# Kernel tuning notes

Measured on AMD Instinct MI355X. Metric: run time of the kernel, lower is better.

Reference implementation:

```python
import jax, jax.numpy as jnp
import numpy as np

N, E, H, C = 50000, 1_600_000, 4, 32
DIN, DE = 128, 32
NEG_SLOPE = 0.2  # PyG GATConv leaky_relu negative_slope default


def setup_inputs() -> dict:
    key = jax.random.key(0)
    ks = jax.random.split(key, 12)
    s = 0.1  # weight scale
    return {
        "x": jax.random.normal(ks[0], (N, DIN), jnp.float32),
        "edge_index": jax.random.randint(ks[1], (2, E), 0, N, jnp.int32),
        "edge_attr": jax.random.normal(ks[2], (E, DE), jnp.float32),
        "W": jax.random.normal(ks[3], (DIN, H * C), jnp.float32) * s,
        "att_src": jax.random.normal(ks[4], (H, C), jnp.float32) * s,
        "att_dst": jax.random.normal(ks[5], (H, C), jnp.float32) * s,
        "lin_edge_W": jax.random.normal(ks[6], (DE, H * C), jnp.float32) * s,
        "att_edge": jax.random.normal(ks[7], (H, C), jnp.float32) * s,
        "bias": jax.random.normal(ks[8], (H * C,), jnp.float32) * s,
        "proj_W": jax.random.normal(ks[9], (H * C, C), jnp.float32) * s,
        "proj_b": jax.random.normal(ks[10], (C,), jnp.float32) * s,
    }


def reference(x, edge_index, edge_attr, W, att_src, att_dst, lin_edge_W,
              att_edge, bias, proj_W, proj_b):
    n = x.shape[0]
    h, c = att_src.shape
    src, dst = edge_index[0], edge_index[1]

    # add self loops; loop edge_attr = mean of incoming edge_attr (PyG fill_value='mean')
    deg = jax.ops.segment_sum(jnp.ones(src.shape, x.dtype), dst, num_segments=n)
    ea_mean = jax.ops.segment_sum(edge_attr, dst, num_segments=n) / jnp.maximum(deg, 1.0)[:, None]
    loop = jnp.arange(n, dtype=src.dtype)
    src = jnp.concatenate([src, loop])
    dst = jnp.concatenate([dst, loop])
    ea = jnp.concatenate([edge_attr, ea_mean], axis=0)

    xl = (x @ W).reshape(n, h, c)                       # [N,H,C]
    a_src = jnp.einsum('nhc,hc->nh', xl, att_src)       # [N,H]
    a_dst = jnp.einsum('nhc,hc->nh', xl, att_dst)
    e = (ea @ lin_edge_W).reshape(-1, h, c)             # [E',H,C]
    a_e = jnp.einsum('ehc,hc->eh', e, att_edge)

    alpha = jax.nn.leaky_relu(a_src[src] + a_dst[dst] + a_e, NEG_SLOPE)  # [E',H]
    amax = jax.lax.stop_gradient(jax.ops.segment_max(alpha, dst, num_segments=n))
    alpha = jnp.exp(alpha - amax[dst])
    denom = jax.ops.segment_sum(alpha, dst, num_segments=n)
    alpha = alpha / (denom[dst] + 1e-16)                # segment softmax over incoming edges

    out = jax.ops.segment_sum(xl[src] * alpha[..., None], dst, num_segments=n)  # [N,H,C]
    out = out.reshape(n, h * c) + bias                  # concat heads + bias
    return out @ proj_W + proj_b                        # concat projection
```

## Files before the change

kernel.cpp:

```cpp
#include <hip/hip_runtime.h>

#define NEG_SLOPE 0.2f

__device__ __forceinline__ float lrelu(float x) { return x > 0.0f ? x : NEG_SLOPE * x; }

__device__ __forceinline__ float bcast(float v, int srcLane) {
  return __int_as_float(__builtin_amdgcn_readlane(__float_as_int(v), srcLane));
}

__device__ __forceinline__ unsigned pack_bf16(float a, float b) {
  unsigned ua = __float_as_uint(a), ub = __float_as_uint(b);
  ua += 0x7fffu + ((ua >> 16) & 1u);
  ub += 0x7fffu + ((ub >> 16) & 1u);
  return (ua >> 16) | (ub & 0xffff0000u);
}
__device__ __forceinline__ float bf16lo(unsigned z) { return __uint_as_float(z << 16); }
__device__ __forceinline__ float bf16hi(unsigned z) { return __uint_as_float(z & 0xffff0000u); }

__global__ void k0_setup(const float* __restrict__ W, const float* __restrict__ proj_W,
                         const float* __restrict__ att_src, const float* __restrict__ att_dst,
                         const float* __restrict__ lin_edge_W, const float* __restrict__ att_edge,
                         const float* __restrict__ bias, const float* __restrict__ proj_b,
                         float* __restrict__ Wz, float* __restrict__ Ws, float* __restrict__ Wd,
                         float* __restrict__ M, float* __restrict__ cproj) {
  int t = blockIdx.x * blockDim.x + threadIdx.x;
  if (t < 16384) {
    int d = t >> 7, o = t & 127;
    int h = o >> 5, jj = o & 31;
    float s = 0.f;
    #pragma unroll
    for (int c = 0; c < 32; ++c)
      s += W[d * 128 + h * 32 + c] * proj_W[(h * 32 + c) * 32 + jj];
    Wz[d * 128 + o] = s;
  } else if (t < 16384 + 512) {
    int idx = t - 16384; int d = idx >> 2, h = idx & 3;
    float s = 0.f;
    #pragma unroll
    for (int c = 0; c < 32; ++c) s += W[d * 128 + h * 32 + c] * att_src[h * 32 + c];
    Ws[d * 4 + h] = s;
  } else if (t < 16384 + 1024) {
    int idx = t - 16384 - 512; int d = idx >> 2, h = idx & 3;
    float s = 0.f;
    #pragma unroll
    for (int c = 0; c < 32; ++c) s += W[d * 128 + h * 32 + c] * att_dst[h * 32 + c];
    Wd[d * 4 + h] = s;
  } else if (t < 16384 + 1024 + 128) {
    int idx = t - 16384 - 1024; int d = idx >> 2, h = idx & 3;
    float s = 0.f;
    #pragma unroll
    for (int c = 0; c < 32; ++c) s += lin_edge_W[d * 128 + h * 32 + c] * att_edge[h * 32 + c];
    M[d * 4 + h] = s;
  } else if (t < 16384 + 1024 + 128 + 32) {
    int jj = t - 16384 - 1024 - 128;
    float s = proj_b[jj];
    #pragma unroll
    for (int k = 0; k < 128; ++k) s += bias[k] * proj_W[k * 32 + jj];
    cproj[jj] = s;
  }
}

__global__ __launch_bounds__(256) void k3_gemm(
    const float* __restrict__ x, const float* __restrict__ Wz,
    const float* __restrict__ Ws, const float* __restrict__ Wd,
    int n, unsigned* __restrict__ Zp, float* __restrict__ a_src, float* __restrict__ a_dst) {
  __shared__ float2 Wl[128 * 64];
  int tid = threadIdx.x;
  for (int idx = tid; idx < 128 * 64; idx += 256) {
    int k = idx >> 6, l = idx & 63;
    Wl[idx] = make_float2(Wz[k * 128 + l], Wz[k * 128 + 64 + l]);
  }
  __syncthreads();
  int lane = tid & 63, wid = tid >> 6;
  float ws0[4], ws1[4], wd0[4], wd1[4];
  #pragma unroll
  for (int h = 0; h < 4; ++h) {
    ws0[h] = Ws[lane * 4 + h];  ws1[h] = Ws[(64 + lane) * 4 + h];
    wd0[h] = Wd[lane * 4 + h];  wd1[h] = Wd[(64 + lane) * 4 + h];
  }
  int gw = blockIdx.x * 4 + wid;
  int nw = gridDim.x * 4;
  for (int base = gw * 4; base < n; base += nw * 4) {
    float xa[4], xb[4];
    #pragma unroll
    for (int u = 0; u < 4; ++u) {
      int node = base + u;
      xa[u] = (node < n) ? x[node * 128 + lane] : 0.0f;
      xb[u] = (node < n) ? x[node * 128 + 64 + lane] : 0.0f;
    }
    float acc0[4] = {0.f, 0.f, 0.f, 0.f}, acc1[4] = {0.f, 0.f, 0.f, 0.f};
    #pragma unroll 16
    for (int k = 0; k < 64; ++k) {
      float2 w = Wl[k * 64 + lane];
      #pragma unroll
      for (int u = 0; u < 4; ++u) {
        float xv = bcast(xa[u], k);
        acc0[u] += xv * w.x; acc1[u] += xv * w.y;
      }
    }
    #pragma unroll 16
    for (int k = 0; k < 64; ++k) {
      float2 w = Wl[(64 + k) * 64 + lane];
      #pragma unroll
      for (int u = 0; u < 4; ++u) {
        float xv = bcast(xb[u], k);
        acc0[u] += xv * w.x; acc1[u] += xv * w.y;
      }
    }
    #pragma unroll
    for (int u = 0; u < 4; ++u) {
      int node = base + u;
      if (node >= n) break;
      Zp[(size_t)node * 64 + lane] = pack_bf16(acc0[u], acc1[u]);
      float ps[4], pd[4];
      #pragma unroll
      for (int h = 0; h < 4; ++h) {
        ps[h] = xa[u] * ws0[h] + xb[u] * ws1[h];
        pd[h] = xa[u] * wd0[h] + xb[u] * wd1[h];
      }
      #pragma unroll
      for (int m = 1; m < 64; m <<= 1) {
        #pragma unroll
        for (int h = 0; h < 4; ++h) {
          ps[h] += __shfl_xor(ps[h], m);
          pd[h] += __shfl_xor(pd[h], m);
        }
      }
      if (lane == 0) {
        *(float4*)&a_src[node * 4] = make_float4(ps[0], ps[1], ps[2], ps[3]);
        *(float4*)&a_dst[node * 4] = make_float4(pd[0], pd[1], pd[2], pd[3]);
      }
    }
  }
}

__global__ __launch_bounds__(256) void k1_edge(
    const int* __restrict__ ei, int E, const float4* __restrict__ ea4,
    const float* __restrict__ Mg,
    const float* __restrict__ a_src, const float* __restrict__ a_dst,
    uint4* __restrict__ we, int* __restrict__ deg, int* __restrict__ rank) {
  int lane = threadIdx.x & 63, wid = threadIdx.x >> 6;
  int j = lane & 7;
  const float4* Mf4 = (const float4*)Mg;
  float4 m0 = Mf4[4 * j + 0], m1 = Mf4[4 * j + 1];
  float4 m2 = Mf4[4 * j + 2], m3 = Mf4[4 * j + 3];
  int perm = 8 * (lane & 7) + (lane >> 3);
  int gw = blockIdx.x * 4 + wid, nw = gridDim.x * 4;
  int ntiles = (E + 63) >> 6;
  for (int tile = gw; tile < ntiles; tile += nw) {
    int T0 = tile << 6;
    size_t fbase = (size_t)T0 * 8;
    float cx = 0.f, cy = 0.f, cz = 0.f, cw = 0.f;
    #pragma unroll
    for (int k = 0; k < 8; ++k) {
      size_t idx = fbase + (size_t)k * 64 + lane;
      float4 v = (idx < (size_t)E * 8) ? ea4[idx] : make_float4(0.f, 0.f, 0.f, 0.f);
      float px = v.x * m0.x + v.y * m1.x + v.z * m2.x + v.w * m3.x;
      float py = v.x * m0.y + v.y * m1.y + v.z * m2.y + v.w * m3.y;
      float pz = v.x * m0.z + v.y * m1.z + v.z * m2.z + v.w * m3.z;
      float pw = v.x * m0.w + v.y * m1.w + v.z * m2.w + v.w * m3.w;
      #pragma unroll
      for (int m = 1; m < 8; m <<= 1) {
        px += __shfl_xor(px, m); py += __shfl_xor(py, m);
        pz += __shfl_xor(pz, m); pw += __shfl_xor(pw, m);
      }
      if (j == k) { cx = px; cy = py; cz = pz; cw = pw; }
    }
    int e = T0 + perm;
    if (e < E) {
      int s = ei[e], d = ei[E + e];
      int rk = atomicAdd(&deg[d], 1);
      float4 as = *(const float4*)&a_src[(size_t)s * 4];
      float4 ad = *(const float4*)&a_dst[(size_t)d * 4];
      float w0 = __expf(lrelu(cx + as.x + ad.x));
      float w1 = __expf(lrelu(cy + as.y + ad.y));
      float w2 = __expf(lrelu(cz + as.z + ad.z));
      float w3 = __expf(lrelu(cw + as.w + ad.w));
      we[e] = make_uint4(pack_bf16(w0, w1), pack_bf16(w2, w3),
                         pack_bf16(cx, cy), pack_bf16(cz, cw));
      rank[e] = rk;
    }
  }
}

__global__ void k2_scan(const int* __restrict__ deg, int n, int* __restrict__ offsets) {
  __shared__ int shw[16];
  __shared__ int shtot;
  int tid = threadIdx.x;
  int lane = tid & 63, wid = tid >> 6;
  int running = 0;
  for (int base = 0; base < n; base += 4096) {
    int i = base + tid * 4;
    int4 v = make_int4(0, 0, 0, 0);
    if (i + 3 < n) v = *(const int4*)&deg[i];
    else {
      if (i < n) v.x = deg[i];
      if (i + 1 < n) v.y = deg[i + 1];
      if (i + 2 < n) v.z = deg[i + 2];
      if (i + 3 < n) v.w = deg[i + 3];
    }
    int tsum = v.x + v.y + v.z + v.w;
    int inc = tsum;
    #pragma unroll
    for (int s = 1; s < 64; s <<= 1) {
      int t = __shfl_up(inc, s);
      if (lane >= s) inc += t;
    }
    if (lane == 63) shw[wid] = inc;
    __syncthreads();
    if (wid == 0) {
      int w = (lane < 16) ? shw[lane] : 0;
      int winc = w;
      #pragma unroll
      for (int s = 1; s < 16; s <<= 1) {
        int t = __shfl_up(winc, s);
        if (lane >= s) winc += t;
      }
      if (lane < 16) shw[lane] = winc - w;
      if (lane == 15) shtot = winc;
    }
    __syncthreads();
    int excl = running + shw[wid] + inc - tsum;
    if (i < n)     offsets[i + 1] = excl + v.x;
    if (i + 1 < n) offsets[i + 2] = excl + v.x + v.y;
    if (i + 2 < n) offsets[i + 3] = excl + v.x + v.y + v.z;
    if (i + 3 < n) offsets[i + 4] = excl + tsum;
    running += shtot;
    __syncthreads();
  }
  if (tid == 0) offsets[0] = 0;
}

__global__ void k4_scatter(const int* __restrict__ ei, int E,
                           const int* __restrict__ rank, const int* __restrict__ offsets,
                           const uint4* __restrict__ we, uint4* __restrict__ csr) {
  int e = blockIdx.x * blockDim.x + threadIdx.x;
  if (e >= E) return;
  int s = ei[e], d = ei[E + e];
  int slot = offsets[d] + rank[e];
  uint4 w = we[e];
  uint4* ent = &csr[(size_t)slot * 2];
  *(int*)ent = s;
  ent[1] = w;
}

__global__ __launch_bounds__(256) void k5_agg(
    const int* __restrict__ offsets, const uint4* __restrict__ csr,
    const unsigned* __restrict__ Zp,
    const float* __restrict__ a_src, const float* __restrict__ a_dst,
    const float* __restrict__ cproj, int n, float* __restrict__ out) {
  __shared__ float4 s_w[4][64];
  __shared__ int    s_s[4][64];
  int tid = threadIdx.x;
  int lane = tid & 63, wid = tid >> 6;
  int gw = blockIdx.x * 4 + wid, nw = gridDim.x * 4;
  int h0 = lane >> 5, j = lane & 31;
  float cp = cproj[j];
  const float* wbase = (const float*)&s_w[wid][0];
  for (int node = gw; node < n; node += nw) {
    int off0 = offsets[node], off1 = offsets[node + 1];
    int dg = off1 - off0;
    float dsx = 0.f, dsy = 0.f, dsz = 0.f, dsw = 0.f;
    float aex = 0.f, aey = 0.f, aez = 0.f, aew = 0.f;
    float agg0 = 0.f, agg1 = 0.f;
    for (int base = off0; base < off1; base += 64) {
      int rem = off1 - base; if (rem > 64) rem = 64;
      if (lane < rem) {
        const uint4* ent = &csr[(size_t)(base + lane) * 2];
        int s = *(const int*)ent;
        uint4 w = ent[1];
        float w0 = bf16lo(w.x), w1 = bf16hi(w.x);
        float w2 = bf16lo(w.y), w3 = bf16hi(w.y);
        dsx += w0; dsy += w1; dsz += w2; dsw += w3;
        aex += bf16lo(w.z); aey += bf16hi(w.z);
        aez += bf16lo(w.w); aew += bf16hi(w.w);
        s_w[wid][lane] = make_float4(w0, w2, w1, w3);
        s_s[wid][lane] = s;
      }
      int jj = 0;
      for (; jj + 4 <= rem; jj += 4) {
        int s0 = s_s[wid][jj], s1 = s_s[wid][jj + 1];
        int s2 = s_s[wid][jj + 2], s3 = s_s[wid][jj + 3];
        unsigned z0 = Zp[(size_t)s0 * 64 + lane];
        unsigned z1 = Zp[(size_t)s1 * 64 + lane];
        unsigned z2 = Zp[(size_t)s2 * 64 + lane];
        unsigned z3 = Zp[(size_t)s3 * 64 + lane];
        float2 w0 = *(const float2*)(wbase + (jj    ) * 4 + 2 * h0);
        float2 w1 = *(const float2*)(wbase + (jj + 1) * 4 + 2 * h0);
        float2 w2 = *(const float2*)(wbase + (jj + 2) * 4 + 2 * h0);
        float2 w3 = *(const float2*)(wbase + (jj + 3) * 4 + 2 * h0);
        agg0 += w0.x * bf16lo(z0) + w1.x * bf16lo(z1) + w2.x * bf16lo(z2) + w3.x * bf16lo(z3);
        agg1 += w0.y * bf16hi(z0) + w1.y * bf16hi(z1) + w2.y * bf16hi(z2) + w3.y * bf16hi(z3);
      }
      for (; jj < rem; ++jj) {
        int s0 = s_s[wid][jj];
        unsigned z0 = Zp[(size_t)s0 * 64 + lane];
        float2 w0 = *(const float2*)(wbase + jj * 4 + 2 * h0);
        agg0 += w0.x * bf16lo(z0);
        agg1 += w0.y * bf16hi(z0);
      }
    }
    #pragma unroll
    for (int m = 1; m < 64; m <<= 1) {
      dsx += __shfl_xor(dsx, m); dsy += __shfl_xor(dsy, m);
      dsz += __shfl_xor(dsz, m); dsw += __shfl_xor(dsw, m);
      aex += __shfl_xor(aex, m); aey += __shfl_xor(aey, m);
      aez += __shfl_xor(aez, m); aew += __shfl_xor(aew, m);
    }
    float invd = 1.0f / (float)(dg > 0 ? dg : 1);
    float4 asn = *(const float4*)&a_src[node * 4];
    float4 ad  = *(const float4*)&a_dst[node * 4];
    float w0 = __expf(lrelu(asn.x + ad.x + aex * invd));
    float w1 = __expf(lrelu(asn.y + ad.y + aey * invd));
    float w2 = __expf(lrelu(asn.z + ad.z + aez * invd));
    float w3 = __expf(lrelu(asn.w + ad.w + aew * invd));
    dsx += w0; dsy += w1; dsz += w2; dsw += w3;
    unsigned zpn = Zp[(size_t)node * 64 + lane];
    float sw0 = h0 ? w1 : w0, sw1 = h0 ? w3 : w2;
    agg0 += sw0 * bf16lo(zpn);
    agg1 += sw1 * bf16hi(zpn);
    float d0 = h0 ? dsy : dsx, d1 = h0 ? dsw : dsz;
    float tt = agg0 / (d0 + 1e-16f) + agg1 / (d1 + 1e-16f);
    tt += __shfl_xor(tt, 32);
    if (lane < 32) out[node * 32 + j] = tt + cp;
  }
}

extern "C" void kernel_launch(void* const* d_in, const int* in_sizes, int n_in,
                              void* d_out, int out_size, void* d_ws, size_t ws_size,
                              hipStream_t stream) {
  const float* x          = (const float*)d_in[0];
  const int*   ei         = (const int*)  d_in[1];
  const float* ea         = (const float*)d_in[2];
  const float* W          = (const float*)d_in[3];
  const float* att_src    = (const float*)d_in[4];
  const float* att_dst    = (const float*)d_in[5];
  const float* lin_edge_W = (const float*)d_in[6];
  const float* att_edge   = (const float*)d_in[7];
  const float* bias       = (const float*)d_in[8];
  const float* proj_W     = (const float*)d_in[9];
  const float* proj_b     = (const float*)d_in[10];
  float* out = (float*)d_out;
  int N = in_sizes[0] / 128;
  int E = in_sizes[1] / 2;

  char* p = (char*)d_ws;
  auto alloc = [&](size_t bytes) {
    char* r = p;
    p += (bytes + 255) & ~(size_t)255;
    return r;
  };
  unsigned* Zp     = (unsigned*)alloc((size_t)N * 64 * 4);
  float* a_src     = (float*)alloc((size_t)N * 4 * 4);
  float* a_dst     = (float*)alloc((size_t)N * 4 * 4);
  int*   deg       = (int*)  alloc((size_t)N * 4);
  int*   offsets   = (int*)  alloc((size_t)(N + 1) * 4);
  int*   rank      = (int*)  alloc((size_t)E * 4);
  uint4* we        = (uint4*)alloc((size_t)E * 16);
  uint4* csr       = (uint4*)alloc((size_t)E * 32);
  float* Wz        = (float*)alloc(128 * 128 * 4);
  float* Ws        = (float*)alloc(128 * 4 * 4);
  float* Wd        = (float*)alloc(128 * 4 * 4);
  float* M         = (float*)alloc(32 * 4 * 4);
  float* cproj     = (float*)alloc(32 * 4);

  hipMemsetAsync(deg, 0, (size_t)N * 4, stream);

  k0_setup<<<69, 256, 0, stream>>>(W, proj_W, att_src, att_dst, lin_edge_W, att_edge,
                                   bias, proj_b, Wz, Ws, Wd, M, cproj);
  k3_gemm<<<512, 256, 0, stream>>>(x, Wz, Ws, Wd, N, Zp, a_src, a_dst);
  k1_edge<<<2048, 256, 0, stream>>>(ei, E, (const float4*)ea, M,
                                    a_src, a_dst, we, deg, rank);
  k2_scan<<<1, 1024, 0, stream>>>(deg, N, offsets);
  k4_scatter<<<(E + 255) / 256, 256, 0, stream>>>(ei, E, rank, offsets, we, csr);
  k5_agg<<<2048, 256, 0, stream>>>(offsets, csr, Zp, a_src, a_dst, cproj, N, out);
}
```

Measured before the change: 558.3 us.

## Count degrees first, then scatter edge weights directly into CSR slots

Result: slower. 609.6 us (+9.2%).

```diff
diff --git a/kernel.cpp b/kernel.cpp
--- a/kernel.cpp
+++ b/kernel.cpp
@@ -133,56 +133,23 @@
   }
 }
 
-__global__ __launch_bounds__(256) void k1_edge(
-    const int* __restrict__ ei, int E, const float4* __restrict__ ea4,
-    const float* __restrict__ Mg,
-    const float* __restrict__ a_src, const float* __restrict__ a_dst,
-    uint4* __restrict__ we, int* __restrict__ deg, int* __restrict__ rank) {
-  int lane = threadIdx.x & 63, wid = threadIdx.x >> 6;
-  int j = lane & 7;
-  const float4* Mf4 = (const float4*)Mg;
-  float4 m0 = Mf4[4 * j + 0], m1 = Mf4[4 * j + 1];
-  float4 m2 = Mf4[4 * j + 2], m3 = Mf4[4 * j + 3];
-  int perm = 8 * (lane & 7) + (lane >> 3);
-  int gw = blockIdx.x * 4 + wid, nw = gridDim.x * 4;
-  int ntiles = (E + 63) >> 6;
-  for (int tile = gw; tile < ntiles; tile += nw) {
-    int T0 = tile << 6;
-    size_t fbase = (size_t)T0 * 8;
-    float cx = 0.f, cy = 0.f, cz = 0.f, cw = 0.f;
-    #pragma unroll
-    for (int k = 0; k < 8; ++k) {
-      size_t idx = fbase + (size_t)k * 64 + lane;
-      float4 v = (idx < (size_t)E * 8) ? ea4[idx] : make_float4(0.f, 0.f, 0.f, 0.f);
-      float px = v.x * m0.x + v.y * m1.x + v.z * m2.x + v.w * m3.x;
-      float py = v.x * m0.y + v.y * m1.y + v.z * m2.y + v.w * m3.y;
-      float pz = v.x * m0.z + v.y * m1.z + v.z * m2.z + v.w * m3.z;
-      float pw = v.x * m0.w + v.y * m1.w + v.z * m2.w + v.w * m3.w;
-      #pragma unroll
-      for (int m = 1; m < 8; m <<= 1) {
-        px += __shfl_xor(px, m); py += __shfl_xor(py, m);
-        pz += __shfl_xor(pz, m); pw += __shfl_xor(pw, m);
-      }
-      if (j == k) { cx = px; cy = py; cz = pz; cw = pw; }
-    }
-    int e = T0 + perm;
-    if (e < E) {
-      int s = ei[e], d = ei[E + e];
-      int rk = atomicAdd(&deg[d], 1);
-      float4 as = *(const float4*)&a_src[(size_t)s * 4];
-      float4 ad = *(const float4*)&a_dst[(size_t)d * 4];
-      float w0 = __expf(lrelu(cx + as.x + ad.x));
-      float w1 = __expf(lrelu(cy + as.y + ad.y));
-      float w2 = __expf(lrelu(cz + as.z + ad.z));
-      float w3 = __expf(lrelu(cw + as.w + ad.w));
-      we[e] = make_uint4(pack_bf16(w0, w1), pack_bf16(w2, w3),
-                         pack_bf16(cx, cy), pack_bf16(cz, cw));
-      rank[e] = rk;
-    }
-  }
-}
-
-__global__ void k2_scan(const int* __restrict__ deg, int n, int* __restrict__ offsets) {
+__global__ __launch_bounds__(256) void kA_deg(const int* __restrict__ ei, int E,
+                                              int* __restrict__ deg) {
+  int t = blockIdx.x * blockDim.x + threadIdx.x;
+  int i = t * 4;
+  if (i + 3 < E) {
+    int4 d = *(const int4*)&ei[E + i];
+    atomicAdd(&deg[d.x], 1);
+    atomicAdd(&deg[d.y], 1);
+    atomicAdd(&deg[d.z], 1);
+    atomicAdd(&deg[d.w], 1);
+  } else {
+    for (int k = i; k < E; ++k) atomicAdd(&deg[ei[E + k]], 1);
+  }
+}
+
+__global__ void k2_scan(const int* __restrict__ deg, int n, int* __restrict__ offsets,
+                        int* __restrict__ cnt) {
   __shared__ int shw[16];
   __shared__ int shtot;
   int tid = threadIdx.x;
@@ -220,27 +187,77 @@
     }
     __syncthreads();
     int excl = running + shw[wid] + inc - tsum;
-    if (i < n)     offsets[i + 1] = excl + v.x;
-    if (i + 1 < n) offsets[i + 2] = excl + v.x + v.y;
-    if (i + 2 < n) offsets[i + 3] = excl + v.x + v.y + v.z;
-    if (i + 3 < n) offsets[i + 4] = excl + tsum;
+    if (i + 3 < n) {
+      *(int4*)&offsets[i + 1] = make_int4(excl + v.x, excl + v.x + v.y,
+                                          excl + v.x + v.y + v.z, excl + tsum);
+      *(int4*)&cnt[i] = make_int4(excl, excl + v.x, excl + v.x + v.y,
+                                  excl + v.x + v.y + v.z);
+    } else {
+      if (i < n)     { offsets[i + 1] = excl + v.x;             cnt[i]     = excl; }
+      if (i + 1 < n) { offsets[i + 2] = excl + v.x + v.y;       cnt[i + 1] = excl + v.x; }
+      if (i + 2 < n) { offsets[i + 3] = excl + v.x + v.y + v.z; cnt[i + 2] = excl + v.x + v.y; }
+      if (i + 3 < n) { offsets[i + 4] = excl + tsum;            cnt[i + 3] = excl + v.x + v.y + v.z; }
+    }
     running += shtot;
     __syncthreads();
   }
   if (tid == 0) offsets[0] = 0;
 }
 
-__global__ void k4_scatter(const int* __restrict__ ei, int E,
-                           const int* __restrict__ rank, const int* __restrict__ offsets,
-                           const uint4* __restrict__ we, uint4* __restrict__ csr) {
-  int e = blockIdx.x * blockDim.x + threadIdx.x;
-  if (e >= E) return;
-  int s = ei[e], d = ei[E + e];
-  int slot = offsets[d] + rank[e];
-  uint4 w = we[e];
-  uint4* ent = &csr[(size_t)slot * 2];
-  *(int*)ent = s;
-  ent[1] = w;
+__global__ __launch_bounds__(256) void k1_edge(
+    const int* __restrict__ ei, int E, const float4* __restrict__ ea4,
+    const float* __restrict__ Mg,
+    const float* __restrict__ a_src, const float* __restrict__ a_dst,
+    int* __restrict__ cnt, uint4* __restrict__ csr) {
+  int lane = threadIdx.x & 63, wid = threadIdx.x >> 6;
+  int j = lane & 7;
+  const float4* Mf4 = (const float4*)Mg;
+  float4 m0 = Mf4[4 * j + 0], m1 = Mf4[4 * j + 1];
+  float4 m2 = Mf4[4 * j + 2], m3 = Mf4[4 * j + 3];
+  int perm = 8 * (lane & 7) + (lane >> 3);
+  int gw = blockIdx.x * 4 + wid, nw = gridDim.x * 4;
+  int ntiles = (E + 63) >> 6;
+  for (int tile = gw; tile < ntiles; tile += nw) {
+    int T0 = tile << 6;
+    int e = T0 + perm;
+    int s = 0, slot = 0;
+    float4 as = make_float4(0.f, 0.f, 0.f, 0.f);
+    float4 ad = make_float4(0.f, 0.f, 0.f, 0.f);
+    if (e < E) {
+      s = ei[e];
+      int d = ei[E + e];
+      slot = atomicAdd(&cnt[d], 1);
+      as = *(const float4*)&a_src[(size_t)s * 4];
+      ad = *(const float4*)&a_dst[(size_t)d * 4];
+    }
+    size_t fbase = (size_t)T0 * 8;
+    float cx = 0.f, cy = 0.f, cz = 0.f, cw = 0.f;
+    #pragma unroll
+    for (int k = 0; k < 8; ++k) {
+      size_t idx = fbase + (size_t)k * 64 + lane;
+      float4 v = (idx < (size_t)E * 8) ? ea4[idx] : make_float4(0.f, 0.f, 0.f, 0.f);
+      float px = v.x * m0.x + v.y * m1.x + v.z * m2.x + v.w * m3.x;
+      float py = v.x * m0.y + v.y * m1.y + v.z * m2.y + v.w * m3.y;
+      float pz = v.x * m0.z + v.y * m1.z + v.z * m2.z + v.w * m3.z;
+      float pw = v.x * m0.w + v.y * m1.w + v.z * m2.w + v.w * m3.w;
+      #pragma unroll
+      for (int m = 1; m < 8; m <<= 1) {
+        px += __shfl_xor(px, m); py += __shfl_xor(py, m);
+        pz += __shfl_xor(pz, m); pw += __shfl_xor(pw, m);
+      }
+      if (j == k) { cx = px; cy = py; cz = pz; cw = pw; }
+    }
+    if (e < E) {
+      float w0 = __expf(lrelu(cx + as.x + ad.x));
+      float w1 = __expf(lrelu(cy + as.y + ad.y));
+      float w2 = __expf(lrelu(cz + as.z + ad.z));
+      float w3 = __expf(lrelu(cw + as.w + ad.w));
+      uint4* ent = &csr[(size_t)slot * 2];
+      *(int*)ent = s;
+      ent[1] = make_uint4(pack_bf16(w0, w1), pack_bf16(w2, w3),
+                          pack_bf16(cx, cy), pack_bf16(cz, cw));
+    }
+  }
 }
 
 __global__ __launch_bounds__(256) void k5_agg(
@@ -353,9 +370,8 @@
   float* a_src     = (float*)alloc((size_t)N * 4 * 4);
   float* a_dst     = (float*)alloc((size_t)N * 4 * 4);
   int*   deg       = (int*)  alloc((size_t)N * 4);
+  int*   cnt       = (int*)  alloc((size_t)N * 4);
   int*   offsets   = (int*)  alloc((size_t)(N + 1) * 4);
-  int*   rank      = (int*)  alloc((size_t)E * 4);
-  uint4* we        = (uint4*)alloc((size_t)E * 16);
   uint4* csr       = (uint4*)alloc((size_t)E * 32);
   float* Wz        = (float*)alloc(128 * 128 * 4);
   float* Ws        = (float*)alloc(128 * 4 * 4);
@@ -368,9 +384,9 @@
   k0_setup<<<69, 256, 0, stream>>>(W, proj_W, att_src, att_dst, lin_edge_W, att_edge,
                                    bias, proj_b, Wz, Ws, Wd, M, cproj);
   k3_gemm<<<512, 256, 0, stream>>>(x, Wz, Ws, Wd, N, Zp, a_src, a_dst);
+  kA_deg<<<(E / 4 + 255) / 256, 256, 0, stream>>>(ei, E, deg);
+  k2_scan<<<1, 1024, 0, stream>>>(deg, N, offsets, cnt);
   k1_edge<<<2048, 256, 0, stream>>>(ei, E, (const float4*)ea, M,
-                                    a_src, a_dst, we, deg, rank);
-  k2_scan<<<1, 1024, 0, stream>>>(deg, N, offsets);
-  k4_scatter<<<(E + 255) / 256, 256, 0, stream>>>(ei, E, rank, offsets, we, csr);
+                                    a_src, a_dst, cnt, csr);
   k5_agg<<<2048, 256, 0, stream>>>(offsets, csr, Zp, a_src, a_dst, cproj, N, out);
 }
```

## Move node projection GEMM to bf16 MFMA and prefetch scan inputs

Applied to the files above, without the earlier changes.

Measured after the change: 531.5 us. 4.8% less time.

```diff
diff --git a/kernel.cpp b/kernel.cpp
--- a/kernel.cpp
+++ b/kernel.cpp
@@ -1,6 +1,9 @@
 #include <hip/hip_runtime.h>
 
 #define NEG_SLOPE 0.2f
+
+typedef float f32x4 __attribute__((ext_vector_type(4)));
+typedef short bf16x8 __attribute__((ext_vector_type(8)));
 
 __device__ __forceinline__ float lrelu(float x) { return x > 0.0f ? x : NEG_SLOPE * x; }
 
@@ -14,6 +17,11 @@
   ub += 0x7fffu + ((ub >> 16) & 1u);
   return (ua >> 16) | (ub & 0xffff0000u);
 }
+__device__ __forceinline__ unsigned short bf16of(float a) {
+  unsigned ua = __float_as_uint(a);
+  ua += 0x7fffu + ((ua >> 16) & 1u);
+  return (unsigned short)(ua >> 16);
+}
 __device__ __forceinline__ float bf16lo(unsigned z) { return __uint_as_float(z << 16); }
 __device__ __forceinline__ float bf16hi(unsigned z) { return __uint_as_float(z & 0xffff0000u); }
 
@@ -21,8 +29,8 @@
                          const float* __restrict__ att_src, const float* __restrict__ att_dst,
                          const float* __restrict__ lin_edge_W, const float* __restrict__ att_edge,
                          const float* __restrict__ bias, const float* __restrict__ proj_b,
-                         float* __restrict__ Wz, float* __restrict__ Ws, float* __restrict__ Wd,
-                         float* __restrict__ M, float* __restrict__ cproj) {
+                         unsigned short* __restrict__ Wzb, float* __restrict__ Ws,
+                         float* __restrict__ Wd, float* __restrict__ M, float* __restrict__ cproj) {
   int t = blockIdx.x * blockDim.x + threadIdx.x;
   if (t < 16384) {
     int d = t >> 7, o = t & 127;
@@ -31,7 +39,7 @@
     #pragma unroll
     for (int c = 0; c < 32; ++c)
       s += W[d * 128 + h * 32 + c] * proj_W[(h * 32 + c) * 32 + jj];
-    Wz[d * 128 + o] = s;
+    Wzb[((d >> 3) * 128 + o) * 8 + (d & 7)] = bf16of(s);
   } else if (t < 16384 + 512) {
     int idx = t - 16384; int d = idx >> 2, h = idx & 3;
     float s = 0.f;
@@ -59,17 +67,10 @@
   }
 }
 
-__global__ __launch_bounds__(256) void k3_gemm(
-    const float* __restrict__ x, const float* __restrict__ Wz,
-    const float* __restrict__ Ws, const float* __restrict__ Wd,
-    int n, unsigned* __restrict__ Zp, float* __restrict__ a_src, float* __restrict__ a_dst) {
-  __shared__ float2 Wl[128 * 64];
+__global__ __launch_bounds__(256) void k3a_att(
+    const float* __restrict__ x, const float* __restrict__ Ws, const float* __restrict__ Wd,
+    int n, float* __restrict__ a_src, float* __restrict__ a_dst) {
   int tid = threadIdx.x;
-  for (int idx = tid; idx < 128 * 64; idx += 256) {
-    int k = idx >> 6, l = idx & 63;
-    Wl[idx] = make_float2(Wz[k * 128 + l], Wz[k * 128 + 64 + l]);
-  }
-  __syncthreads();
   int lane = tid & 63, wid = tid >> 6;
   float ws0[4], ws1[4], wd0[4], wd1[4];
   #pragma unroll
@@ -84,33 +85,13 @@
     #pragma unroll
     for (int u = 0; u < 4; ++u) {
       int node = base + u;
-      xa[u] = (node < n) ? x[node * 128 + lane] : 0.0f;
-      xb[u] = (node < n) ? x[node * 128 + 64 + lane] : 0.0f;
-    }
-    float acc0[4] = {0.f, 0.f, 0.f, 0.f}, acc1[4] = {0.f, 0.f, 0.f, 0.f};
-    #pragma unroll 16
-    for (int k = 0; k < 64; ++k) {
-      float2 w = Wl[k * 64 + lane];
-      #pragma unroll
-      for (int u = 0; u < 4; ++u) {
-        float xv = bcast(xa[u], k);
-        acc0[u] += xv * w.x; acc1[u] += xv * w.y;
-      }
-    }
-    #pragma unroll 16
-    for (int k = 0; k < 64; ++k) {
-      float2 w = Wl[(64 + k) * 64 + lane];
-      #pragma unroll
-      for (int u = 0; u < 4; ++u) {
-        float xv = bcast(xb[u], k);
-        acc0[u] += xv * w.x; acc1[u] += xv * w.y;
-      }
+      xa[u] = (node < n) ? x[(size_t)node * 128 + lane] : 0.0f;
+      xb[u] = (node < n) ? x[(size_t)node * 128 + 64 + lane] : 0.0f;
     }
     #pragma unroll
     for (int u = 0; u < 4; ++u) {
       int node = base + u;
       if (node >= n) break;
-      Zp[(size_t)node * 64 + lane] = pack_bf16(acc0[u], acc1[u]);
       float ps[4], pd[4];
       #pragma unroll
       for (int h = 0; h < 4; ++h) {
@@ -129,6 +110,53 @@
         *(float4*)&a_src[node * 4] = make_float4(ps[0], ps[1], ps[2], ps[3]);
         *(float4*)&a_dst[node * 4] = make_float4(pd[0], pd[1], pd[2], pd[3]);
       }
+    }
+  }
+}
+
+__global__ __launch_bounds__(256) void k3b_gemm(
+    const float* __restrict__ x, const unsigned short* __restrict__ Wzb,
+    int n, unsigned* __restrict__ Zp) {
+  __shared__ __align__(16) unsigned short WzL[16384];
+  int tid = threadIdx.x;
+  #pragma unroll
+  for (int i = 0; i < 8; ++i)
+    *(uint4*)&WzL[(i * 256 + tid) * 8] = *(const uint4*)&Wzb[(i * 256 + tid) * 8];
+  __syncthreads();
+  int lane = tid & 63, wid = tid >> 6;
+  int rgrp = lane >> 4, rl = lane & 15;
+  int r0 = blockIdx.x * 64 + wid * 16;
+  if (r0 >= n) return;
+  int row = r0 + rl; if (row >= n) row = n - 1;
+  const float* xr = x + (size_t)row * 128 + rgrp * 8;
+  bf16x8 a[4];
+  #pragma unroll
+  for (int q = 0; q < 4; ++q) {
+    float4 v0 = *(const float4*)(xr + q * 32);
+    float4 v1 = *(const float4*)(xr + q * 32 + 4);
+    union { unsigned u[4]; bf16x8 v; } fa;
+    fa.u[0] = pack_bf16(v0.x, v0.y); fa.u[1] = pack_bf16(v0.z, v0.w);
+    fa.u[2] = pack_bf16(v1.x, v1.y); fa.u[3] = pack_bf16(v1.z, v1.w);
+    a[q] = fa.v;
+  }
+  f32x4 acc[8];
+  #pragma unroll
+  for (int t = 0; t < 8; ++t) acc[t] = (f32x4){0.f, 0.f, 0.f, 0.f};
+  #pragma unroll
+  for (int q = 0; q < 4; ++q) {
+    #pragma unroll
+    for (int t = 0; t < 8; ++t) {
+      bf16x8 b = *(const bf16x8*)&WzL[((q * 4 + rgrp) * 128 + t * 16 + rl) * 8];
+      acc[t] = __builtin_amdgcn_mfma_f32_16x16x32_bf16(a[q], b, acc[t], 0, 0, 0);
+    }
+  }
+  #pragma unroll
+  for (int t = 0; t < 4; ++t) {
+    #pragma unroll
+    for (int r = 0; r < 4; ++r) {
+      int rr = r0 + rgrp * 4 + r;
+      if (rr < n)
+        Zp[(size_t)rr * 64 + t * 16 + rl] = pack_bf16(acc[t][r], acc[t + 4][r]);
     }
   }
 }
@@ -182,50 +210,64 @@
   }
 }
 
-__global__ void k2_scan(const int* __restrict__ deg, int n, int* __restrict__ offsets) {
+__global__ __launch_bounds__(1024) void k2_scan(const int* __restrict__ deg, int n,
+                                                int* __restrict__ offsets) {
   __shared__ int shw[16];
   __shared__ int shtot;
   int tid = threadIdx.x;
   int lane = tid & 63, wid = tid >> 6;
+  int nch = (n + 4095) >> 12;
+  int4 v[16];
+  #pragma unroll
+  for (int c = 0; c < 16; ++c) {
+    if (c < nch) {
+      int i = c * 4096 + tid * 4;
+      int4 t = make_int4(0, 0, 0, 0);
+      if (i + 3 < n) t = *(const int4*)&deg[i];
+      else {
+        if (i < n) t.x = deg[i];
+        if (i + 1 < n) t.y = deg[i + 1];
+        if (i + 2 < n) t.z = deg[i + 2];
+        if (i + 3 < n) t.w = deg[i + 3];
+      }
+      v[c] = t;
+    }
+  }
   int running = 0;
-  for (int base = 0; base < n; base += 4096) {
-    int i = base + tid * 4;
-    int4 v = make_int4(0, 0, 0, 0);
-    if (i + 3 < n) v = *(const int4*)&deg[i];
-    else {
-      if (i < n) v.x = deg[i];
-      if (i + 1 < n) v.y = deg[i + 1];
-      if (i + 2 < n) v.z = deg[i + 2];
-      if (i + 3 < n) v.w = deg[i + 3];
-    }
-    int tsum = v.x + v.y + v.z + v.w;
-    int inc = tsum;
-    #pragma unroll
-    for (int s = 1; s < 64; s <<= 1) {
-      int t = __shfl_up(inc, s);
-      if (lane >= s) inc += t;
-    }
-    if (lane == 63) shw[wid] = inc;
-    __syncthreads();
-    if (wid == 0) {
-      int w = (lane < 16) ? shw[lane] : 0;
-      int winc = w;
+  #pragma unroll
+  for (int c = 0; c < 16; ++c) {
+    if (c < nch) {
+      int i = c * 4096 + tid * 4;
+      int4 t = v[c];
+      int tsum = t.x + t.y + t.z + t.w;
+      int inc = tsum;
       #pragma unroll
-      for (int s = 1; s < 16; s <<= 1) {
-        int t = __shfl_up(winc, s);
-        if (lane >= s) winc += t;
-      }
-      if (lane < 16) shw[lane] = winc - w;
-      if (lane == 15) shtot = winc;
-    }
-    __syncthreads();
-    int excl = running + shw[wid] + inc - tsum;
-    if (i < n)     offsets[i + 1] = excl + v.x;
-    if (i + 1 < n) offsets[i + 2] = excl + v.x + v.y;
-    if (i + 2 < n) offsets[i + 3] = excl + v.x + v.y + v.z;
-    if (i + 3 < n) offsets[i + 4] = excl + tsum;
-    running += shtot;
-    __syncthreads();
+      for (int s = 1; s < 64; s <<= 1) {
+        int q = __shfl_up(inc, s);
+        if (lane >= s) inc += q;
+      }
+      if (lane == 63) shw[wid] = inc;
+      __syncthreads();
+      if (wid == 0) {
+        int w = (lane < 16) ? shw[lane] : 0;
+        int winc = w;
+        #pragma unroll
+        for (int s = 1; s < 16; s <<= 1) {
+          int q = __shfl_up(winc, s);
+          if (lane >= s) winc += q;
+        }
+        if (lane < 16) shw[lane] = winc - w;
+        if (lane == 15) shtot = winc;
+      }
+      __syncthreads();
+      int excl = running + shw[wid] + inc - tsum;
+      if (i < n)     offsets[i + 1] = excl + t.x;
+      if (i + 1 < n) offsets[i + 2] = excl + t.x + t.y;
+      if (i + 2 < n) offsets[i + 3] = excl + t.x + t.y + t.z;
+      if (i + 3 < n) offsets[i + 4] = excl + tsum;
+      running += shtot;
+      __syncthreads();
+    }
   }
   if (tid == 0) offsets[0] = 0;
 }
@@ -349,25 +391,26 @@
     p += (bytes + 255) & ~(size_t)255;
     return r;
   };
-  unsigned* Zp     = (unsigned*)alloc((size_t)N * 64 * 4);
-  float* a_src     = (float*)alloc((size_t)N * 4 * 4);
-  float* a_dst     = (float*)alloc((size_t)N * 4 * 4);
-  int*   deg       = (int*)  alloc((size_t)N * 4);
-  int*   offsets   = (int*)  alloc((size_t)(N + 1) * 4);
-  int*   rank      = (int*)  alloc((size_t)E * 4);
-  uint4* we        = (uint4*)alloc((size_t)E * 16);
-  uint4* csr       = (uint4*)alloc((size_t)E * 32);
-  float* Wz        = (float*)alloc(128 * 128 * 4);
-  float* Ws        = (float*)alloc(128 * 4 * 4);
-  float* Wd        = (float*)alloc(128 * 4 * 4);
-  float* M         = (float*)alloc(32 * 4 * 4);
-  float* cproj     = (float*)alloc(32 * 4);
+  unsigned* Zp          = (unsigned*)alloc((size_t)N * 64 * 4);
+  float* a_src          = (float*)alloc((size_t)N * 4 * 4);
+  float* a_dst          = (float*)alloc((size_t)N * 4 * 4);
+  int*   deg            = (int*)  alloc((size_t)N * 4);
+  int*   offsets        = (int*)  alloc((size_t)(N + 1) * 4);
+  int*   rank           = (int*)  alloc((size_t)E * 4);
+  uint4* we             = (uint4*)alloc((size_t)E * 16);
+  uint4* csr            = (uint4*)alloc((size_t)E * 32);
+  unsigned short* Wzb   = (unsigned short*)alloc(16384 * 2);
+  float* Ws             = (float*)alloc(128 * 4 * 4);
+  float* Wd             = (float*)alloc(128 * 4 * 4);
+  float* M              = (float*)alloc(32 * 4 * 4);
+  float* cproj          = (float*)alloc(32 * 4);
 
   hipMemsetAsync(deg, 0, (size_t)N * 4, stream);
 
   k0_setup<<<69, 256, 0, stream>>>(W, proj_W, att_src, att_dst, lin_edge_W, att_edge,
-                                   bias, proj_b, Wz, Ws, Wd, M, cproj);
-  k3_gemm<<<512, 256, 0, stream>>>(x, Wz, Ws, Wd, N, Zp, a_src, a_dst);
+                                   bias, proj_b, Wzb, Ws, Wd, M, cproj);
+  k3a_att<<<512, 256, 0, stream>>>(x, Ws, Wd, N, a_src, a_dst);
+  k3b_gemm<<<(N + 63) / 64, 256, 0, stream>>>(x, Wzb, N, Zp);
   k1_edge<<<2048, 256, 0, stream>>>(ei, E, (const float4*)ea, M,
                                     a_src, a_dst, we, deg, rank);
   k2_scan<<<1, 1024, 0, stream>>>(deg, N, offsets);
```
